# Kernel tuning notes

Hardware: AMD Instinct MI355X
Metric: run time of the kernel (lower is better)

Reference implementation:

```python
import jax, jax.numpy as jnp
import numpy as np

N = 50000   # nodes
E = 200000  # edges
F = 128     # node feat dim
M = 128     # memory dim
FE = 64     # edge feat dim
H = 256     # hidden dim
T = 16      # time encoding dim
O = 64      # output dim
L = 2       # attention layers
NH = 4      # heads
HD = H // NH
SCALE = float(np.sqrt(HD))


def time_enc(t, w, phi):
    # Time2Vec: linear first channel, sinusoidal rest
    wt = t[..., None] * w + phi
    return jnp.concatenate([wt[..., :1], jnp.sin(wt[..., 1:])], axis=-1)


def layer_norm(x, g, b, eps=1e-5):
    m = x.mean(-1, keepdims=True)
    v = jnp.mean((x - m) ** 2, axis=-1, keepdims=True)
    return (x - m) / jnp.sqrt(v + eps) * g + b


def setup_inputs() -> dict:
    key = jax.random.key(0)
    ks = jax.random.split(key, 12)
    s = 0.05  # weight scale for numeric sanity
    return {
        "node_feat": jax.random.normal(ks[0], (N, F), jnp.float32),
        "memory": jax.random.normal(ks[1], (N, M), jnp.float32),
        "edge_index": jax.random.randint(ks[2], (2, E), 0, N),
        "edge_feat": jax.random.normal(ks[3], (E, FE), jnp.float32),
        "edge_times": jax.random.uniform(ks[4], (E,), jnp.float32),
        "in_w": jax.random.normal(ks[5], (H, F + M), jnp.float32) * s,
        "in_b": jnp.zeros((H,), jnp.float32),
        "te_w": jax.random.normal(ks[6], (L, T), jnp.float32),
        "te_phi": jnp.zeros((L, T), jnp.float32),
        "wq_w": jax.random.normal(ks[7], (L, H, H + T), jnp.float32) * s,
        "wq_b": jnp.zeros((L, H), jnp.float32),
        "wk_w": jax.random.normal(ks[8], (L, H, H + FE + T), jnp.float32) * s,
        "wk_b": jnp.zeros((L, H), jnp.float32),
        "wv_w": jax.random.normal(ks[9], (L, H, H + FE + T), jnp.float32) * s,
        "wv_b": jnp.zeros((L, H), jnp.float32),
        "attn_ln_w": jnp.ones((L, H), jnp.float32),
        "attn_ln_b": jnp.zeros((L, H), jnp.float32),
        "ln_w": jnp.ones((L, H), jnp.float32),
        "ln_b": jnp.zeros((L, H), jnp.float32),
        "out_w": jax.random.normal(ks[10], (O, H), jnp.float32) * s,
        "out_b": jnp.zeros((O,), jnp.float32),
    }


def reference(node_feat, memory, edge_index, edge_feat, edge_times,
              in_w, in_b, te_w, te_phi, wq_w, wq_b, wk_w, wk_b, wv_w, wv_b,
              attn_ln_w, attn_ln_b, ln_w, ln_b, out_w, out_b):
    src, dst = edge_index[0], edge_index[1]
    td = 0.0 - edge_times  # query_time = 0.0 (default)
    h = jnp.concatenate([node_feat, memory], axis=-1) @ in_w.T + in_b  # (N, H)
    for l in range(L):
        tenc = time_enc(td, te_w[l], te_phi[l])                       # (E, T)
        h_dst = h[dst]                                                # (E, H)
        msg = jnp.concatenate([h[src], edge_feat, tenc], axis=-1)     # (E, H+FE+T)
        q_te = time_enc(jnp.zeros((N,), h.dtype), te_w[l], te_phi[l]) # (N, T)
        # faithful to source: E > max(dst_ids) so branch is dst_feat[dst_ids]
        q_in = jnp.concatenate([h_dst[dst], q_te[dst]], axis=-1)      # (E, H+T)
        Q = (q_in @ wq_w[l].T + wq_b[l]).reshape(E, NH, HD)
        K = (msg @ wk_w[l].T + wk_b[l]).reshape(E, NH, HD)
        V = msg @ wv_w[l].T + wv_b[l]                                 # (E, H)
        scores = (Q * K).sum(-1) / SCALE                              # (E, NH)
        attn = jnp.exp(jnp.clip(scores, -5.0, 5.0))
        af = attn.mean(-1, keepdims=True)                             # (E, 1)
        agg = jax.ops.segment_sum(V * af, dst, num_segments=N)        # (N, H)
        nrm = jax.ops.segment_sum(af, dst, num_segments=N)            # (N, 1)
        h_new = layer_norm(agg / (nrm + 1e-8), attn_ln_w[l], attn_ln_b[l])
        h = layer_norm(h + h_new, ln_w[l], ln_b[l])
    return jax.nn.gelu(h @ out_w.T + out_b, approximate=False)        # (N, O)
```

## Files before the change

### kernel.cpp

```cpp
#include <hip/hip_runtime.h>
#include <hip/hip_bf16.h>
#include <math.h>

#define NN 50000
#define EE 200000

typedef __bf16 bf16x8 __attribute__((ext_vector_type(8)));
typedef __bf16 bf16x4 __attribute__((ext_vector_type(4)));
typedef __bf16 bf16x2 __attribute__((ext_vector_type(2)));
typedef float f32x4 __attribute__((ext_vector_type(4)));

static __device__ __forceinline__ bf16x8 ld8(const __bf16* p) {
  return *reinterpret_cast<const bf16x8*>(p);
}
static __device__ __forceinline__ bf16x4 ld4(const __bf16* p) {
  return *reinterpret_cast<const bf16x4*>(p);
}
static __device__ __forceinline__ bf16x8 zero8() {
  bf16x8 z;
  #pragma unroll
  for (int j = 0; j < 8; ++j) z[j] = (__bf16)0.0f;
  return z;
}


__global__ __launch_bounds__(256) void k_prep(const float* __restrict__ inw,
                                              const float* __restrict__ wq,
                                              const float* __restrict__ wk,
                                              const float* __restrict__ wvw,
                                              const float* __restrict__ ow,
                                              const float* __restrict__ ef,
                                              const float* __restrict__ tim,
                                              const float* __restrict__ tew,
                                              const float* __restrict__ teph,
                                              const float* __restrict__ wqb,
                                              const int* __restrict__ ei,
                                              __bf16* __restrict__ cinw,
                                              __bf16* __restrict__ cwq,
                                              __bf16* __restrict__ cwk,
                                              __bf16* __restrict__ cwv,
                                              __bf16* __restrict__ cow,
                                              __bf16* __restrict__ twk,
                                              __bf16* __restrict__ aux,
                                              float* __restrict__ cq,
                                              int* __restrict__ cnt) {
  const int b = blockIdx.x;
  if (b < 2208) {
    int i = b * 256 + threadIdx.x;
    if (i < 65536) cinw[i] = (__bf16)inw[i];
    else if (i < 204800) { int j = i - 65536;  cwq[j] = (__bf16)wq[j]; }
    else if (i < 376832) { int j = i - 204800; cwk[j] = (__bf16)wk[j]; }
    else if (i < 548864) { int j = i - 376832; cwv[j] = (__bf16)wvw[j]; }
    else if (i < 565248) { int j = i - 548864; cow[j] = (__bf16)ow[j]; }
  } else if (b < 2400) {
    int i = (b - 2208) * 256 + threadIdx.x;
    int l = i / 24576, r = i % 24576;
    int h = r / 6144, jd = r % 6144;
    int j = jd / 64, d = jd % 64;
    __bf16 v = (__bf16)0.0f;
    if (j < 80) v = (__bf16)wk[((size_t)l * 256 + h * 64 + d) * 336 + 256 + j];
    twk[i] = v;
  } else if (b < 52400) {
    int lane = threadIdx.x & 63;
    int wv = threadIdx.x >> 6;
    int e = (b - 2400) * 4 + wv;
    __bf16* row = aux + (size_t)e * 96;
    row[lane] = (__bf16)ef[(size_t)e * 64 + lane];
    if (lane >= 16 && lane < 32) row[64 + lane] = (__bf16)0.0f;
  } else if (b < 52402) {
    int l = b - 52400;
    int n = threadIdx.x;
    const float* wq_l = wq + (size_t)l * 256 * 272;
    const float* teph_l = teph + l * 16;
    float s = wqb[l * 256 + n];
    for (int t = 0; t < 16; ++t) {
      float ph = teph_l[t];
      float q = (t == 0) ? ph : sinf(ph);
      s += q * wq_l[(size_t)n * 272 + 256 + t];
    }
    cq[l * 256 + n] = s;
  } else if (b < 64902) {
    int idx = (b - 52402) * 256 + threadIdx.x;
    int e = idx >> 4, t = idx & 15;
    float td = -tim[e];
    float wt = td * tew[t] + teph[t];
    float v = (t == 0) ? wt : __sinf(wt);
    aux[(size_t)e * 96 + 64 + t] = (__bf16)v;
  } else {
    int e = (b - 64902) * 256 + threadIdx.x;
    if (e < EE) atomicAdd(&cnt[ei[EE + e]], 1);
  }
}

__global__ __launch_bounds__(256) void k_blksum(const int* __restrict__ wp, int* __restrict__ bsum) {
  __shared__ int red[256];
  int i = blockIdx.x * 256 + threadIdx.x;
  int v = (i < NN) ? wp[i] : 0;
  red[threadIdx.x] = v;
  __syncthreads();
  for (int off = 128; off > 0; off >>= 1) {
    if (threadIdx.x < off) red[threadIdx.x] += red[threadIdx.x + off];
    __syncthreads();
  }
  if (threadIdx.x == 0) bsum[blockIdx.x] = red[0];
}

__global__ __launch_bounds__(256) void k_scanb(int* __restrict__ bsum, int nb) {
  __shared__ int s[256];
  int t = threadIdx.x;
  int v = (t < nb) ? bsum[t] : 0;
  s[t] = v;
  __syncthreads();
  for (int off = 1; off < 256; off <<= 1) {
    int u = (t >= off) ? s[t - off] : 0;
    __syncthreads();
    s[t] += u;
    __syncthreads();
  }
  if (t < nb) bsum[t] = s[t] - v;
}

__global__ __launch_bounds__(256) void k_scanc(int* __restrict__ wp,
                                               const int* __restrict__ bsum,
                                               int* __restrict__ rowptr) {
  __shared__ int s[256];
  int i = blockIdx.x * 256 + threadIdx.x;
  int t = threadIdx.x;
  int v = (i < NN) ? wp[i] : 0;
  s[t] = v;
  __syncthreads();
  for (int off = 1; off < 256; off <<= 1) {
    int u = (t >= off) ? s[t - off] : 0;
    __syncthreads();
    s[t] += u;
    __syncthreads();
  }
  int excl = s[t] - v + bsum[blockIdx.x];
  if (i < NN) { rowptr[i] = excl; wp[i] = excl; }
  if (i == 0) rowptr[NN] = EE;
}

__global__ __launch_bounds__(256) void k_fill(const int* __restrict__ ei,
                                              int* __restrict__ wp,
                                              int* __restrict__ bucket) {
  int e = blockIdx.x * 256 + threadIdx.x;
  if (e < EE) {
    int d = ei[EE + e];
    int pos = atomicAdd(&wp[d], 1);
    bucket[pos] = e;
  }
}

__global__ __launch_bounds__(256) void k_auxte(const float* __restrict__ tim,
                                               const float* __restrict__ tew_l,
                                               const float* __restrict__ teph_l,
                                               __bf16* __restrict__ aux) {
  int idx = blockIdx.x * 256 + threadIdx.x;
  int e = idx >> 4, t = idx & 15;
  float td = -tim[e];
  float wt = td * tew_l[t] + teph_l[t];
  float v = (t == 0) ? wt : __sinf(wt);
  aux[(size_t)e * 96 + 64 + t] = (__bf16)v;
}


__global__ __launch_bounds__(256) void k_h0(const float* __restrict__ nf,
                                            const float* __restrict__ mem,
                                            const __bf16* __restrict__ w,
                                            const float* __restrict__ bias,
                                            __bf16* __restrict__ hb) {
  __shared__ __bf16 As[64][264];
  const int t = threadIdx.x;
  const int lane = t & 63;
  const int wv = t >> 6;
  const int c = lane & 15, g = lane >> 4;
  const int row0 = blockIdx.x * 64;
  const int colbase = wv * 64;

  {
    const int col4 = t & 63;
    const int rb = t >> 6;
    const bool useMem = (col4 >= 32);
    const int coff = (useMem ? (col4 - 32) : col4) * 4;
    const float* basep = useMem ? mem : nf;
    #pragma unroll
    for (int i = 0; i < 16; ++i) {
      const int row = rb + i * 4;
      int grow = row0 + row; if (grow >= NN) grow = NN - 1;
      f32x4 v = *reinterpret_cast<const f32x4*>(basep + (size_t)grow * 128 + coff);
      bf16x4 bv;
      bv[0] = (__bf16)v[0]; bv[1] = (__bf16)v[1];
      bv[2] = (__bf16)v[2]; bv[3] = (__bf16)v[3];
      *reinterpret_cast<bf16x4*>(&As[row][col4 * 4]) = bv;
    }
  }
  __syncthreads();

  const __bf16* Bp[4];
  #pragma unroll
  for (int ct = 0; ct < 4; ++ct)
    Bp[ct] = w + (size_t)(colbase + ct * 16 + c) * 256;

  f32x4 acc[4][4];
  #pragma unroll
  for (int rt = 0; rt < 4; ++rt)
    for (int ct = 0; ct < 4; ++ct)
      for (int r = 0; r < 4; ++r) acc[rt][ct][r] = 0.0f;

  #pragma unroll
  for (int ks = 0; ks < 8; ++ks) {
    const int k = ks * 32 + g * 8;
    bf16x8 a[4], b[4];
    #pragma unroll
    for (int rt = 0; rt < 4; ++rt)
      a[rt] = *reinterpret_cast<const bf16x8*>(&As[rt * 16 + c][k]);
    #pragma unroll
    for (int ct = 0; ct < 4; ++ct) b[ct] = ld8(Bp[ct] + k);
    #pragma unroll
    for (int rt = 0; rt < 4; ++rt)
      #pragma unroll
      for (int ct = 0; ct < 4; ++ct)
        acc[rt][ct] = __builtin_amdgcn_mfma_f32_16x16x32_bf16(a[rt], b[ct], acc[rt][ct], 0, 0, 0);
  }
  __syncthreads();

  #pragma unroll
  for (int ct = 0; ct < 4; ++ct) {
    const float bv = bias[colbase + ct * 16 + c];
    #pragma unroll
    for (int rt = 0; rt < 4; ++rt)
      #pragma unroll
      for (int rr = 0; rr < 4; ++rr)
        As[rt * 16 + g * 4 + rr][colbase + ct * 16 + c] = (__bf16)(acc[rt][ct][rr] + bv);
  }
  #pragma unroll
  for (int i = 0; i < 8; ++i) {
    const int r = i * 8 + (lane >> 3);
    const int ck = lane & 7;
    bf16x8 v = *reinterpret_cast<const bf16x8*>(&As[r][colbase + ck * 8]);
    const int row = row0 + r;
    if (row < NN)
      *reinterpret_cast<bf16x8*>(hb + (size_t)row * 256 + colbase + ck * 8) = v;
  }
}


__global__ __launch_bounds__(256, 2) void k_qkn(const __bf16* __restrict__ hb,
                                                const __bf16* __restrict__ wq_l,
                                                const __bf16* __restrict__ wk_l,
                                                const float* __restrict__ cq,
                                                const float* __restrict__ bk_l,
                                                const __bf16* __restrict__ twk_l,
                                                __bf16* __restrict__ Qn,
                                                __bf16* __restrict__ Kn,
                                                __bf16* __restrict__ G) {
  __shared__ __bf16 As[64][264];
  __shared__ __bf16 tile[4][64][84];
  const int lane = threadIdx.x & 63;
  const int wv = threadIdx.x >> 6;
  const int c = lane & 15, g = lane >> 4;
  const int row0 = blockIdx.x * 64;
  const int colbase = wv * 64;

  {
    #pragma unroll
    for (int i = 0; i < 8; ++i) {
      const int cc = threadIdx.x + i * 256;
      const int row = cc >> 5;
      const int col8 = cc & 31;
      int grow = row0 + row; if (grow >= NN) grow = NN - 1;
      *reinterpret_cast<bf16x8*>(&As[row][col8 * 8]) =
          ld8(hb + (size_t)grow * 256 + col8 * 8);
    }
  }
  __syncthreads();

  f32x4 acc[4][4];

  #pragma unroll
  for (int rt = 0; rt < 4; ++rt)
    for (int ct = 0; ct < 4; ++ct)
      for (int r = 0; r < 4; ++r) acc[rt][ct][r] = 0.0f;
  {
    const __bf16* Bp[4];
    #pragma unroll
    for (int ct = 0; ct < 4; ++ct)
      Bp[ct] = wq_l + (size_t)(colbase + ct * 16 + c) * 272;
    #pragma unroll
    for (int ks = 0; ks < 8; ++ks) {
      const int k = ks * 32 + g * 8;
      bf16x8 a[4], b[4];
      #pragma unroll
      for (int rt = 0; rt < 4; ++rt)
        a[rt] = *reinterpret_cast<const bf16x8*>(&As[rt * 16 + c][k]);
      #pragma unroll
      for (int ct = 0; ct < 4; ++ct) b[ct] = ld8(Bp[ct] + k);
      #pragma unroll
      for (int rt = 0; rt < 4; ++rt)
        #pragma unroll
        for (int ct = 0; ct < 4; ++ct)
          acc[rt][ct] = __builtin_amdgcn_mfma_f32_16x16x32_bf16(a[rt], b[ct], acc[rt][ct], 0, 0, 0);
    }
  }
  #pragma unroll
  for (int ct = 0; ct < 4; ++ct) {
    const float cqv = cq[colbase + ct * 16 + c];
    #pragma unroll
    for (int rt = 0; rt < 4; ++rt)
      #pragma unroll
      for (int rr = 0; rr < 4; ++rr)
        tile[wv][rt * 16 + g * 4 + rr][ct * 16 + c] = (__bf16)(acc[rt][ct][rr] + cqv);
  }
  #pragma unroll
  for (int i = 0; i < 8; ++i) {
    const int r = i * 8 + (lane >> 3);
    const int ck = lane & 7;
    bf16x8 v = *reinterpret_cast<const bf16x8*>(&tile[wv][r][ck * 8]);
    const int row = row0 + r;
    if (row < NN)
      *reinterpret_cast<bf16x8*>(Qn + (size_t)row * 256 + colbase + ck * 8) = v;
  }

  {
    f32x4 accg[4][5];
    #pragma unroll
    for (int rt = 0; rt < 4; ++rt)
      for (int ct = 0; ct < 5; ++ct)
        for (int r = 0; r < 4; ++r) accg[rt][ct][r] = 0.0f;
    const __bf16* Bp[5];
    #pragma unroll
    for (int ct = 0; ct < 5; ++ct)
      Bp[ct] = twk_l + (size_t)wv * 6144 + (size_t)(ct * 16 + c) * 64;
    #pragma unroll
    for (int ks = 0; ks < 2; ++ks) {
      const int k = ks * 32 + g * 8;
      bf16x8 a[4], b[5];
      #pragma unroll
      for (int rt = 0; rt < 4; ++rt)
        a[rt] = *reinterpret_cast<const bf16x8*>(&tile[wv][rt * 16 + c][k]);
      #pragma unroll
      for (int ct = 0; ct < 5; ++ct) b[ct] = ld8(Bp[ct] + k);
      #pragma unroll
      for (int rt = 0; rt < 4; ++rt)
        #pragma unroll
        for (int ct = 0; ct < 5; ++ct)
          accg[rt][ct] = __builtin_amdgcn_mfma_f32_16x16x32_bf16(a[rt], b[ct], accg[rt][ct], 0, 0, 0);
    }
    #pragma unroll
    for (int ct = 0; ct < 5; ++ct) {
      #pragma unroll
      for (int rt = 0; rt < 4; ++rt)
        #pragma unroll
        for (int rr = 0; rr < 4; ++rr)
          tile[wv][rt * 16 + g * 4 + rr][ct * 16 + c] = (__bf16)accg[rt][ct][rr];
    }
    #pragma unroll
    for (int i = 0; i < 10; ++i) {
      const int idx = i * 64 + lane;
      const int r = idx / 10;
      const int ck = idx % 10;
      bf16x8 v = *reinterpret_cast<const bf16x8*>(&tile[wv][r][ck * 8]);
      const int row = row0 + r;
      if (row < NN)
        *reinterpret_cast<bf16x8*>(G + (size_t)row * 320 + wv * 80 + ck * 8) = v;
    }
  }

  #pragma unroll
  for (int rt = 0; rt < 4; ++rt)
    for (int ct = 0; ct < 4; ++ct)
      for (int r = 0; r < 4; ++r) acc[rt][ct][r] = 0.0f;
  {
    const __bf16* Bp[4];
    #pragma unroll
    for (int ct = 0; ct < 4; ++ct)
      Bp[ct] = wk_l + (size_t)(colbase + ct * 16 + c) * 336;
    #pragma unroll
    for (int ks = 0; ks < 8; ++ks) {
      const int k = ks * 32 + g * 8;
      bf16x8 a[4], b[4];
      #pragma unroll
      for (int rt = 0; rt < 4; ++rt)
        a[rt] = *reinterpret_cast<const bf16x8*>(&As[rt * 16 + c][k]);
      #pragma unroll
      for (int ct = 0; ct < 4; ++ct) b[ct] = ld8(Bp[ct] + k);
      #pragma unroll
      for (int rt = 0; rt < 4; ++rt)
        #pragma unroll
        for (int ct = 0; ct < 4; ++ct)
          acc[rt][ct] = __builtin_amdgcn_mfma_f32_16x16x32_bf16(a[rt], b[ct], acc[rt][ct], 0, 0, 0);
    }
  }
  #pragma unroll
  for (int ct = 0; ct < 4; ++ct) {
    const float bkv = bk_l[colbase + ct * 16 + c];
    #pragma unroll
    for (int rt = 0; rt < 4; ++rt)
      #pragma unroll
      for (int rr = 0; rr < 4; ++rr)
        tile[wv][rt * 16 + g * 4 + rr][ct * 16 + c] = (__bf16)(acc[rt][ct][rr] + bkv);
  }
  #pragma unroll
  for (int i = 0; i < 8; ++i) {
    const int r = i * 8 + (lane >> 3);
    const int ck = lane & 7;
    bf16x8 v = *reinterpret_cast<const bf16x8*>(&tile[wv][r][ck * 8]);
    const int row = row0 + r;
    if (row < NN)
      *reinterpret_cast<bf16x8*>(Kn + (size_t)row * 256 + colbase + ck * 8) = v;
  }
}


__global__ __launch_bounds__(256, 4) void k_sagg(const __bf16* __restrict__ hb,
                                                 const __bf16* __restrict__ aux,
                                                 const __bf16* __restrict__ G,
                                                 const __bf16* __restrict__ Qn,
                                                 const __bf16* __restrict__ Kn,
                                                 const int* __restrict__ ei,
                                                 const int* __restrict__ rowptr,
                                                 const int* __restrict__ bucket,
                                                 __bf16* __restrict__ maggH,
                                                 __bf16* __restrict__ maggX,
                                                 float* __restrict__ sfac) {
  const int lane = threadIdx.x & 63;
  const int wv = threadIdx.x >> 6;
  const int node = blockIdx.x * 4 + wv;
  const int beg = rowptr[node], end = rowptr[node + 1];
  const int c = lane & 15;
  const int grp = lane >> 4;

  float aH[4] = {0, 0, 0, 0};
  float aXv[4] = {0, 0, 0, 0};
  float aXs = 0.0f;
  float nrm = 0.0f;

  if (beg < end) {
    const int iq = ei[EE + node];
    const __bf16* Qr = Qn + (size_t)iq * 256;
    const __bf16* Gr = G + (size_t)iq * 320;

    bf16x4 qv = ld4(Qr + lane * 4);
    bf16x4 gv = ld4(Gr + grp * 80 + c * 4);
    const float gs = (float)Gr[grp * 80 + 64 + c];

    int e = bucket[beg];
    int s = ei[e];
    bf16x4 kv = ld4(Kn + (size_t)s * 256 + lane * 4);
    bf16x4 hv = ld4(hb + (size_t)s * 256 + lane * 4);
    bf16x4 av = ld4(aux + (size_t)e * 96 + c * 4);
    float as = (float)aux[(size_t)e * 96 + 64 + c];

    for (int i = beg; i < end; ++i) {
      const int en = (i + 1 < end) ? bucket[i + 1] : e;
      const int sn = ei[en];
      bf16x4 kv_n = ld4(Kn + (size_t)sn * 256 + lane * 4);
      bf16x4 hv_n = ld4(hb + (size_t)sn * 256 + lane * 4);
      bf16x4 av_n = ld4(aux + (size_t)en * 96 + c * 4);
      float as_n = (float)aux[(size_t)en * 96 + 64 + c];

      float p = gs * as;
      #pragma unroll
      for (int j = 0; j < 4; ++j) {
        p += (float)qv[j] * (float)kv[j];
        p += (float)gv[j] * (float)av[j];
      }
      p += __shfl_xor(p, 1, 64);
      p += __shfl_xor(p, 2, 64);
      p += __shfl_xor(p, 4, 64);
      p += __shfl_xor(p, 8, 64);
      float sc = fminf(5.0f, fmaxf(-5.0f, p * 0.125f));
      float ex = __expf(sc);
      ex += __shfl_xor(ex, 16, 64);
      ex += __shfl_xor(ex, 32, 64);
      const float a = ex * 0.25f;

      nrm += a;
      #pragma unroll
      for (int j = 0; j < 4; ++j) aH[j] += a * (float)hv[j];
      if (grp == 0) {
        #pragma unroll
        for (int j = 0; j < 4; ++j) aXv[j] += a * (float)av[j];
      } else if (grp == 1) {
        aXs += a * as;
      }
      kv = kv_n; hv = hv_n; av = av_n; as = as_n; e = en;
    }
  }

  const float inv = 1.0f / (nrm + 1e-8f);
  bf16x4 oh;
  #pragma unroll
  for (int j = 0; j < 4; ++j) oh[j] = (__bf16)(aH[j] * inv);
  *reinterpret_cast<bf16x4*>(maggH + (size_t)node * 256 + lane * 4) = oh;
  if (grp == 0) {
    bf16x4 ox;
    #pragma unroll
    for (int j = 0; j < 4; ++j) ox[j] = (__bf16)(aXv[j] * inv);
    *reinterpret_cast<bf16x4*>(maggX + (size_t)node * 96 + c * 4) = ox;
  } else if (grp == 1) {
    maggX[(size_t)node * 96 + 64 + c] = (__bf16)(aXs * inv);
  } else if (grp == 2) {
    maggX[(size_t)node * 96 + 80 + c] = (__bf16)0.0f;
  }
  if (lane == 0) sfac[node] = nrm * inv;
}


__global__ __launch_bounds__(256, 4) void k_score3(const __bf16* __restrict__ aux,
                                                   const __bf16* __restrict__ G,
                                                   const __bf16* __restrict__ Qn,
                                                   const __bf16* __restrict__ Kn,
                                                   const int* __restrict__ ei,
                                                   const int* __restrict__ rowptr,
                                                   const int* __restrict__ bucket,
                                                   float* __restrict__ af) {
  const int lane = threadIdx.x & 63;
  const int wv = threadIdx.x >> 6;
  const int node = blockIdx.x * 4 + wv;
  const int beg = rowptr[node], end = rowptr[node + 1];
  const int c = lane & 15;
  const int grp = lane >> 4;

  if (beg < end) {
    const int iq = ei[EE + node];
    const __bf16* Qr = Qn + (size_t)iq * 256;
    const __bf16* Gr = G + (size_t)iq * 320;

    bf16x4 qv = ld4(Qr + lane * 4);
    bf16x4 gv = ld4(Gr + grp * 80 + c * 4);
    const float gs = (float)Gr[grp * 80 + 64 + c];

    int e = bucket[beg];
    int s = ei[e];
    for (int i = beg; i < end; ++i) {
      const int en = (i + 1 < end) ? bucket[i + 1] : e;
      const int sn = ei[en];
      bf16x4 kv = ld4(Kn + (size_t)s * 256 + lane * 4);
      bf16x4 av = ld4(aux + (size_t)e * 96 + c * 4);
      float as = (float)aux[(size_t)e * 96 + 64 + c];

      float p = gs * as;
      #pragma unroll
      for (int j = 0; j < 4; ++j) {
        p += (float)qv[j] * (float)kv[j];
        p += (float)gv[j] * (float)av[j];
      }
      p += __shfl_xor(p, 1, 64);
      p += __shfl_xor(p, 2, 64);
      p += __shfl_xor(p, 4, 64);
      p += __shfl_xor(p, 8, 64);
      float sc = fminf(5.0f, fmaxf(-5.0f, p * 0.125f));
      float ex = __expf(sc);
      ex += __shfl_xor(ex, 16, 64);
      ex += __shfl_xor(ex, 32, 64);
      if (lane == 0) af[e] = ex * 0.25f;
      e = en; s = sn;
    }
  }
}

__global__ __launch_bounds__(256, 4) void k_magg(const __bf16* __restrict__ hb,
                                                 const __bf16* __restrict__ aux,
                                                 const int* __restrict__ ei,
                                                 const int* __restrict__ rowptr,
                                                 const int* __restrict__ bucket,
                                                 const float* __restrict__ af,
                                                 __bf16* __restrict__ maggH,
                                                 __bf16* __restrict__ maggX,
                                                 float* __restrict__ sfac) {
  const int lane = threadIdx.x & 63;
  const int wv = threadIdx.x >> 6;
  const int node = blockIdx.x * 4 + wv;
  const int beg = rowptr[node], end = rowptr[node + 1];

  float aH[4] = {0, 0, 0, 0};
  float aX[2] = {0, 0};
  float nrm = 0.0f;
  if (beg < end) {
    int e = bucket[beg];
    float a = af[e];
    int s = ei[e];
    for (int i = beg; i < end; ++i) {
      const int en = (i + 1 < end) ? bucket[i + 1] : e;
      const float an = af[en];
      const int sn = ei[en];
      bf16x4 hv = ld4(hb + (size_t)s * 256 + lane * 4);
      #pragma unroll
      for (int j = 0; j < 4; ++j) aH[j] += a * (float)hv[j];
      if (lane < 48) {
        bf16x2 xv = *reinterpret_cast<const bf16x2*>(aux + (size_t)e * 96 + lane * 2);
        aX[0] += a * (float)xv[0];
        aX[1] += a * (float)xv[1];
      }
      nrm += a;
      e = en; a = an; s = sn;
    }
  }
  const float inv = 1.0f / (nrm + 1e-8f);
  bf16x4 oh;
  #pragma unroll
  for (int j = 0; j < 4; ++j) oh[j] = (__bf16)(aH[j] * inv);
  *reinterpret_cast<bf16x4*>(maggH + (size_t)node * 256 + lane * 4) = oh;
  if (lane < 48) {
    bf16x2 ox;
    ox[0] = (__bf16)(aX[0] * inv);
    ox[1] = (__bf16)(aX[1] * inv);
    *reinterpret_cast<bf16x2*>(maggX + (size_t)node * 96 + lane * 2) = ox;
  }
  if (lane == 0) sfac[node] = nrm * inv;
}


__global__ __launch_bounds__(256, 3) void k_vnorm(const __bf16* __restrict__ maggH,
                                                  const __bf16* __restrict__ maggX,
                                                  const float* __restrict__ sfac,
                                                  const __bf16* __restrict__ wv_l,
                                                  const float* __restrict__ bv_l,
                                                  __bf16* __restrict__ hb,
                                                  const float* __restrict__ aw,
                                                  const float* __restrict__ ab,
                                                  const float* __restrict__ lw,
                                                  const float* __restrict__ lb) {
  __shared__ __bf16 tile[4][64][68];
  __shared__ float redA[64][4];
  __shared__ float redB[64][4];
  const int lane = threadIdx.x & 63;
  const int wv = threadIdx.x >> 6;
  const int c = lane & 15, g = lane >> 4;
  const int row0 = blockIdx.x * 64;
  const int colbase = wv * 64;

  #pragma unroll
  for (int i = 0; i < 8; ++i) {
    const int r = i * 8 + (lane >> 3);
    const int ck = lane & 7;
    int row = row0 + r; if (row >= NN) row = NN - 1;
    *reinterpret_cast<bf16x8*>(&tile[wv][r][ck * 8]) =
        ld8(hb + (size_t)row * 256 + colbase + ck * 8);
  }

  const __bf16* AH[4];
  const __bf16* AX[4];
  const __bf16* Bp[4];
  #pragma unroll
  for (int rt = 0; rt < 4; ++rt) {
    int r = row0 + rt * 16 + c; if (r >= NN) r = NN - 1;
    AH[rt] = maggH + (size_t)r * 256;
    AX[rt] = maggX + (size_t)r * 96;
  }
  #pragma unroll
  for (int ct = 0; ct < 4; ++ct)
    Bp[ct] = wv_l + (size_t)(colbase + ct * 16 + c) * 336;

  f32x4 acc[4][4];
  #pragma unroll
  for (int rt = 0; rt < 4; ++rt)
    for (int ct = 0; ct < 4; ++ct)
      for (int r = 0; r < 4; ++r) acc[rt][ct][r] = 0.0f;

  for (int ks = 0; ks < 8; ++ks) {
    const int k = ks * 32 + g * 8;
    bf16x8 a[4], b[4];
    #pragma unroll
    for (int rt = 0; rt < 4; ++rt) a[rt] = ld8(AH[rt] + k);
    #pragma unroll
    for (int ct = 0; ct < 4; ++ct) b[ct] = ld8(Bp[ct] + k);
    #pragma unroll
    for (int rt = 0; rt < 4; ++rt)
      #pragma unroll
      for (int ct = 0; ct < 4; ++ct)
        acc[rt][ct] = __builtin_amdgcn_mfma_f32_16x16x32_bf16(a[rt], b[ct], acc[rt][ct], 0, 0, 0);
  }
  const bf16x8 bz = zero8();
  for (int ks = 0; ks < 3; ++ks) {
    const int kk = ks * 32 + g * 8;
    bf16x8 a[4], b[4];
    #pragma unroll
    for (int rt = 0; rt < 4; ++rt) a[rt] = ld8(AX[rt] + kk);
    #pragma unroll
    for (int ct = 0; ct < 4; ++ct)
      b[ct] = (kk < 80) ? ld8(Bp[ct] + 256 + kk) : bz;
    #pragma unroll
    for (int rt = 0; rt < 4; ++rt)
      #pragma unroll
      for (int ct = 0; ct < 4; ++ct)
        acc[rt][ct] = __builtin_amdgcn_mfma_f32_16x16x32_bf16(a[rt], b[ct], acc[rt][ct], 0, 0, 0);
  }

  float sf[4][4];
  #pragma unroll
  for (int rt = 0; rt < 4; ++rt)
    #pragma unroll
    for (int rr = 0; rr < 4; ++rr) {
      int row = row0 + rt * 16 + g * 4 + rr; if (row >= NN) row = NN - 1;
      sf[rt][rr] = sfac[row];
    }
  float bvv[4], awv[4], abv[4], lwv[4], lbv[4];
  #pragma unroll
  for (int ct = 0; ct < 4; ++ct) {
    const int col = colbase + ct * 16 + c;
    bvv[ct] = bv_l[col];
    awv[ct] = aw[col]; abv[ct] = ab[col];
    lwv[ct] = lw[col]; lbv[ct] = lb[col];
  }
  #pragma unroll
  for (int rt = 0; rt < 4; ++rt)
    #pragma unroll
    for (int ct = 0; ct < 4; ++ct)
      #pragma unroll
      for (int rr = 0; rr < 4; ++rr)
        acc[rt][ct][rr] += sf[rt][rr] * bvv[ct];

  float s1[4][4];
  #pragma unroll
  for (int rt = 0; rt < 4; ++rt)
    #pragma unroll
    for (int rr = 0; rr < 4; ++rr) {
      float s = 0.0f;
      #pragma unroll
      for (int ct = 0; ct < 4; ++ct) s += acc[rt][ct][rr];
      #pragma unroll
      for (int m = 1; m < 16; m <<= 1) s += __shfl_xor(s, m, 64);
      s1[rt][rr] = s;
    }
  if (c == 0)
    #pragma unroll
    for (int rt = 0; rt < 4; ++rt)
      #pragma unroll
      for (int rr = 0; rr < 4; ++rr)
        redA[rt * 16 + g * 4 + rr][wv] = s1[rt][rr];
  __syncthreads();
  float mean1[4][4];
  #pragma unroll
  for (int rt = 0; rt < 4; ++rt)
    #pragma unroll
    for (int rr = 0; rr < 4; ++rr) {
      const int r = rt * 16 + g * 4 + rr;
      mean1[rt][rr] = (redA[r][0] + redA[r][1] + redA[r][2] + redA[r][3]) * (1.0f / 256.0f);
    }
  #pragma unroll
  for (int rt = 0; rt < 4; ++rt)
    #pragma unroll
    for (int rr = 0; rr < 4; ++rr) {
      float q = 0.0f;
      #pragma unroll
      for (int ct = 0; ct < 4; ++ct) {
        float d = acc[rt][ct][rr] - mean1[rt][rr];
        q += d * d;
      }
      #pragma unroll
      for (int m = 1; m < 16; m <<= 1) q += __shfl_xor(q, m, 64);
      s1[rt][rr] = q;
    }
  if (c == 0)
    #pragma unroll
    for (int rt = 0; rt < 4; ++rt)
      #pragma unroll
      for (int rr = 0; rr < 4; ++rr)
        redB[rt * 16 + g * 4 + rr][wv] = s1[rt][rr];
  __syncthreads();
  float rstd1[4][4];
  #pragma unroll
  for (int rt = 0; rt < 4; ++rt)
    #pragma unroll
    for (int rr = 0; rr < 4; ++rr) {
      const int r = rt * 16 + g * 4 + rr;
      float v = (redB[r][0] + redB[r][1] + redB[r][2] + redB[r][3]) * (1.0f / 256.0f);
      rstd1[rt][rr] = rsqrtf(v + 1e-5f);
    }

  #pragma unroll
  for (int rt = 0; rt < 4; ++rt)
    #pragma unroll
    for (int rr = 0; rr < 4; ++rr) {
      const int r = rt * 16 + g * 4 + rr;
      float s = 0.0f;
      #pragma unroll
      for (int ct = 0; ct < 4; ++ct) {
        float hbv = (float)tile[wv][r][ct * 16 + c];
        float y = hbv + (acc[rt][ct][rr] - mean1[rt][rr]) * rstd1[rt][rr] * awv[ct] + abv[ct];
        acc[rt][ct][rr] = y;
        s += y;
      }
      #pragma unroll
      for (int m = 1; m < 16; m <<= 1) s += __shfl_xor(s, m, 64);
      s1[rt][rr] = s;
    }
  if (c == 0)
    #pragma unroll
    for (int rt = 0; rt < 4; ++rt)
      #pragma unroll
      for (int rr = 0; rr < 4; ++rr)
        redA[rt * 16 + g * 4 + rr][wv] = s1[rt][rr];
  __syncthreads();
  float mean2[4][4];
  #pragma unroll
  for (int rt = 0; rt < 4; ++rt)
    #pragma unroll
    for (int rr = 0; rr < 4; ++rr) {
      const int r = rt * 16 + g * 4 + rr;
      mean2[rt][rr] = (redA[r][0] + redA[r][1] + redA[r][2] + redA[r][3]) * (1.0f / 256.0f);
    }
  #pragma unroll
  for (int rt = 0; rt < 4; ++rt)
    #pragma unroll
    for (int rr = 0; rr < 4; ++rr) {
      float q = 0.0f;
      #pragma unroll
      for (int ct = 0; ct < 4; ++ct) {
        float d = acc[rt][ct][rr] - mean2[rt][rr];
        q += d * d;
      }
      #pragma unroll
      for (int m = 1; m < 16; m <<= 1) q += __shfl_xor(q, m, 64);
      s1[rt][rr] = q;
    }
  if (c == 0)
    #pragma unroll
    for (int rt = 0; rt < 4; ++rt)
      #pragma unroll
      for (int rr = 0; rr < 4; ++rr)
        redB[rt * 16 + g * 4 + rr][wv] = s1[rt][rr];
  __syncthreads();
  #pragma unroll
  for (int rt = 0; rt < 4; ++rt)
    #pragma unroll
    for (int rr = 0; rr < 4; ++rr) {
      const int r = rt * 16 + g * 4 + rr;
      float v = (redB[r][0] + redB[r][1] + redB[r][2] + redB[r][3]) * (1.0f / 256.0f);
      const float rstd2 = rsqrtf(v + 1e-5f);
      #pragma unroll
      for (int ct = 0; ct < 4; ++ct)
        tile[wv][r][ct * 16 + c] =
            (__bf16)((acc[rt][ct][rr] - mean2[rt][rr]) * rstd2 * lwv[ct] + lbv[ct]);
    }

  #pragma unroll
  for (int i = 0; i < 8; ++i) {
    const int r = i * 8 + (lane >> 3);
    const int ck = lane & 7;
    bf16x8 v = *reinterpret_cast<const bf16x8*>(&tile[wv][r][ck * 8]);
    const int row = row0 + r;
    if (row < NN)
      *reinterpret_cast<bf16x8*>(hb + (size_t)row * 256 + colbase + ck * 8) = v;
  }
}


__global__ __launch_bounds__(256, 4) void k_out(const __bf16* __restrict__ hb,
                                                const __bf16* __restrict__ ow,
                                                const float* __restrict__ ob,
                                                float* __restrict__ out) {
  const int lane = threadIdx.x & 63;
  const int wv = threadIdx.x >> 6;
  const int c = lane & 15, g = lane >> 4;
  const int row0 = blockIdx.x * 64 + wv * 16;

  int r = row0 + c; if (r >= NN) r = NN - 1;
  const __bf16* Ar = hb + (size_t)r * 256;
  const __bf16* Bp[4];
  #pragma unroll
  for (int ct = 0; ct < 4; ++ct)
    Bp[ct] = ow + (size_t)(ct * 16 + c) * 256;

  f32x4 acc[4];
  #pragma unroll
  for (int ct = 0; ct < 4; ++ct)
    for (int rr = 0; rr < 4; ++rr) acc[ct][rr] = 0.0f;

  for (int ks = 0; ks < 8; ++ks) {
    const int k = ks * 32 + g * 8;
    bf16x8 a = ld8(Ar + k);
    bf16x8 b[4];
    #pragma unroll
    for (int ct = 0; ct < 4; ++ct) b[ct] = ld8(Bp[ct] + k);
    #pragma unroll
    for (int ct = 0; ct < 4; ++ct)
      acc[ct] = __builtin_amdgcn_mfma_f32_16x16x32_bf16(a, b[ct], acc[ct], 0, 0, 0);
  }
  #pragma unroll
  for (int ct = 0; ct < 4; ++ct) {
    const int col = ct * 16 + c;
    const float bv = ob[col];
    #pragma unroll
    for (int rr = 0; rr < 4; ++rr) {
      const int row = row0 + g * 4 + rr;
      if (row < NN) {
        float x = acc[ct][rr] + bv;
        out[(size_t)row * 64 + col] = 0.5f * x * (1.0f + erff(x * 0.70710678118654752f));
      }
    }
  }
}


extern "C" void kernel_launch(void* const* d_in, const int* in_sizes, int n_in,
                              void* d_out, int out_size, void* d_ws, size_t ws_size,
                              hipStream_t stream) {
  (void)in_sizes; (void)n_in; (void)out_size;
  const float* nf   = (const float*)d_in[0];
  const float* mem  = (const float*)d_in[1];
  const int*   ei   = (const int*)d_in[2];
  const float* ef   = (const float*)d_in[3];
  const float* tim  = (const float*)d_in[4];
  const float* inw  = (const float*)d_in[5];
  const float* inb  = (const float*)d_in[6];
  const float* tew  = (const float*)d_in[7];
  const float* teph = (const float*)d_in[8];
  const float* wq   = (const float*)d_in[9];
  const float* wqb  = (const float*)d_in[10];
  const float* wk   = (const float*)d_in[11];
  const float* wkb  = (const float*)d_in[12];
  const float* wvw  = (const float*)d_in[13];
  const float* wvb  = (const float*)d_in[14];
  const float* alw  = (const float*)d_in[15];
  const float* alb  = (const float*)d_in[16];
  const float* lnw  = (const float*)d_in[17];
  const float* lnb  = (const float*)d_in[18];
  const float* ow   = (const float*)d_in[19];
  const float* ob   = (const float*)d_in[20];
  float* out = (float*)d_out;

  char* ws = (char*)d_ws;
  const bool big = ws_size >= 186700000ULL;

  __bf16* hb    = (__bf16*)(ws + 0);
  __bf16* aux   = (__bf16*)(ws + 25600000);
  __bf16* Qn    = (__bf16*)(ws + 64000000);
  __bf16* Kn    = (__bf16*)(ws + 89600000);
  __bf16* G     = (__bf16*)(ws + 115200000);
  __bf16* maggH = (__bf16*)(ws + (big ? 147200000 : 115200000));
  __bf16* maggX = (__bf16*)(ws + (big ? 172800000 : 140800000));
  const size_t o_tail = big ? 182400000 : 150400000;
  float*  sfac  = (float*) (ws + o_tail);
  float*  af    = (float*) (ws + o_tail + 200000);
  int*    rowptr= (int*)   (ws + o_tail + 1800000);
  int*    wp    = (int*)   (ws + o_tail + 2000192);
  int*    bucket= (int*)   (ws + o_tail + 2200192);
  float*  cq    = (float*) (ws + o_tail + 3000192);
  int*    bsum  = (int*)   (ws + o_tail + 3002240);
  __bf16* cinw  = (__bf16*)(ws + o_tail + 3003264);
  __bf16* cwq   = (__bf16*)(ws + o_tail + 3134336);
  __bf16* cwk   = (__bf16*)(ws + o_tail + 3412864);
  __bf16* cwv   = (__bf16*)(ws + o_tail + 3756928);
  __bf16* cow   = (__bf16*)(ws + o_tail + 4100992);
  __bf16* twk   = (__bf16*)(ws + o_tail + 4133760);

  const int NB = (NN + 255) / 256;
  hipMemsetAsync(wp, 0, NN * 4, stream);
  k_prep<<<65684, 256, 0, stream>>>(inw, wq, wk, wvw, ow, ef, tim, tew, teph, wqb, ei,
                                    cinw, cwq, cwk, cwv, cow, twk, aux, cq, wp);
  k_blksum<<<NB, 256, 0, stream>>>(wp, bsum);
  k_scanb<<<1, 256, 0, stream>>>(bsum, NB);
  k_scanc<<<NB, 256, 0, stream>>>(wp, bsum, rowptr);
  k_fill<<<(EE + 255) / 256, 256, 0, stream>>>(ei, wp, bucket);

  k_h0<<<(NN + 63) / 64, 256, 0, stream>>>(nf, mem, cinw, inb, hb);

  for (int l = 0; l < 2; ++l) {
    const __bf16* wq_l = cwq + (size_t)l * 256 * 272;
    const __bf16* wk_l = cwk + (size_t)l * 256 * 336;
    const __bf16* wv_l = cwv + (size_t)l * 256 * 336;
    if (l > 0)
      k_auxte<<<EE * 16 / 256, 256, 0, stream>>>(tim, tew + l * 16, teph + l * 16, aux);
    k_qkn<<<(NN + 63) / 64, 256, 0, stream>>>(hb, wq_l, wk_l, cq + l * 256, wkb + l * 256,
                                              twk + (size_t)l * 24576, Qn, Kn, G);
    if (big) {
      k_sagg<<<NN / 4, 256, 0, stream>>>(hb, aux, G, Qn, Kn, ei, rowptr, bucket,
                                         maggH, maggX, sfac);
    } else {
      k_score3<<<NN / 4, 256, 0, stream>>>(aux, G, Qn, Kn, ei, rowptr, bucket, af);
      k_magg<<<NN / 4, 256, 0, stream>>>(hb, aux, ei, rowptr, bucket, af, maggH, maggX, sfac);
    }
    k_vnorm<<<(NN + 63) / 64, 256, 0, stream>>>(maggH, maggX, sfac, wv_l, wvb + l * 256, hb,
                                                alw + l * 256, alb + l * 256,
                                                lnw + l * 256, lnb + l * 256);
  }
  k_out<<<(NN + 63) / 64, 256, 0, stream>>>(hb, cow, ob, out);
}
```

Baseline: 566.7 us.

## Unroll edge aggregation by four and fuse output projection into final vnorm

The per-node edge loop in k_sagg now handles four edges per iteration. All gathers for those four edges are issued together and their shuffle reductions are interleaved, which exposes more memory-level parallelism than the previous one-ahead prefetch. The occupancy hint on k_sagg's launch bounds is dropped. The final output projection with GELU is fused into the last-layer k_vnorm, reading the normalized tile from shared memory; this removes the hb write-back, a kernel launch and the re-read. The trade-off is higher register pressure in k_sagg and wasted work on padded edges for nodes with low degree.

```diff
diff --git a/kernel.cpp b/kernel.cpp
--- a/kernel.cpp
+++ b/kernel.cpp
@@ -412,17 +412,17 @@
 }
 
 
-__global__ __launch_bounds__(256, 4) void k_sagg(const __bf16* __restrict__ hb,
-                                                 const __bf16* __restrict__ aux,
-                                                 const __bf16* __restrict__ G,
-                                                 const __bf16* __restrict__ Qn,
-                                                 const __bf16* __restrict__ Kn,
-                                                 const int* __restrict__ ei,
-                                                 const int* __restrict__ rowptr,
-                                                 const int* __restrict__ bucket,
-                                                 __bf16* __restrict__ maggH,
-                                                 __bf16* __restrict__ maggX,
-                                                 float* __restrict__ sfac) {
+__global__ __launch_bounds__(256) void k_sagg(const __bf16* __restrict__ hb,
+                                              const __bf16* __restrict__ aux,
+                                              const __bf16* __restrict__ G,
+                                              const __bf16* __restrict__ Qn,
+                                              const __bf16* __restrict__ Kn,
+                                              const int* __restrict__ ei,
+                                              const int* __restrict__ rowptr,
+                                              const int* __restrict__ bucket,
+                                              __bf16* __restrict__ maggH,
+                                              __bf16* __restrict__ maggX,
+                                              float* __restrict__ sfac) {
   const int lane = threadIdx.x & 63;
   const int wv = threadIdx.x >> 6;
   const int node = blockIdx.x * 4 + wv;
@@ -444,47 +444,78 @@
     bf16x4 gv = ld4(Gr + grp * 80 + c * 4);
     const float gs = (float)Gr[grp * 80 + 64 + c];
 
-    int e = bucket[beg];
-    int s = ei[e];
-    bf16x4 kv = ld4(Kn + (size_t)s * 256 + lane * 4);
-    bf16x4 hv = ld4(hb + (size_t)s * 256 + lane * 4);
-    bf16x4 av = ld4(aux + (size_t)e * 96 + c * 4);
-    float as = (float)aux[(size_t)e * 96 + 64 + c];
-
-    for (int i = beg; i < end; ++i) {
-      const int en = (i + 1 < end) ? bucket[i + 1] : e;
-      const int sn = ei[en];
-      bf16x4 kv_n = ld4(Kn + (size_t)sn * 256 + lane * 4);
-      bf16x4 hv_n = ld4(hb + (size_t)sn * 256 + lane * 4);
-      bf16x4 av_n = ld4(aux + (size_t)en * 96 + c * 4);
-      float as_n = (float)aux[(size_t)en * 96 + 64 + c];
-
-      float p = gs * as;
+    for (int base = beg; base < end; base += 4) {
+      const int rem = end - base;
+      const int iA = base;
+      const int iB = base + ((1 < rem) ? 1 : 0);
+      const int iC = base + ((2 < rem) ? 2 : 0);
+      const int iD = base + ((3 < rem) ? 3 : 0);
+      const int eA = bucket[iA], eB = bucket[iB], eC = bucket[iC], eD = bucket[iD];
+      const int sA = ei[eA], sB = ei[eB], sC = ei[eC], sD = ei[eD];
+
+      bf16x4 kvA = ld4(Kn + (size_t)sA * 256 + lane * 4);
+      bf16x4 kvB = ld4(Kn + (size_t)sB * 256 + lane * 4);
+      bf16x4 kvC = ld4(Kn + (size_t)sC * 256 + lane * 4);
+      bf16x4 kvD = ld4(Kn + (size_t)sD * 256 + lane * 4);
+      bf16x4 hvA = ld4(hb + (size_t)sA * 256 + lane * 4);
+      bf16x4 hvB = ld4(hb + (size_t)sB * 256 + lane * 4);
+      bf16x4 hvC = ld4(hb + (size_t)sC * 256 + lane * 4);
+      bf16x4 hvD = ld4(hb + (size_t)sD * 256 + lane * 4);
+      bf16x4 avA = ld4(aux + (size_t)eA * 96 + c * 4);
+      bf16x4 avB = ld4(aux + (size_t)eB * 96 + c * 4);
+      bf16x4 avC = ld4(aux + (size_t)eC * 96 + c * 4);
+      bf16x4 avD = ld4(aux + (size_t)eD * 96 + c * 4);
+      const float asA = (float)aux[(size_t)eA * 96 + 64 + c];
+      const float asB = (float)aux[(size_t)eB * 96 + 64 + c];
+      const float asC = (float)aux[(size_t)eC * 96 + 64 + c];
+      const float asD = (float)aux[(size_t)eD * 96 + 64 + c];
+
+      float pA = gs * asA, pB = gs * asB, pC = gs * asC, pD = gs * asD;
       #pragma unroll
       for (int j = 0; j < 4; ++j) {
-        p += (float)qv[j] * (float)kv[j];
-        p += (float)gv[j] * (float)av[j];
+        const float qj = (float)qv[j], gj = (float)gv[j];
+        pA += qj * (float)kvA[j] + gj * (float)avA[j];
+        pB += qj * (float)kvB[j] + gj * (float)avB[j];
+        pC += qj * (float)kvC[j] + gj * (float)avC[j];
+        pD += qj * (float)kvD[j] + gj * (float)avD[j];
       }
-      p += __shfl_xor(p, 1, 64);
-      p += __shfl_xor(p, 2, 64);
-      p += __shfl_xor(p, 4, 64);
-      p += __shfl_xor(p, 8, 64);
-      float sc = fminf(5.0f, fmaxf(-5.0f, p * 0.125f));
-      float ex = __expf(sc);
-      ex += __shfl_xor(ex, 16, 64);
-      ex += __shfl_xor(ex, 32, 64);
-      const float a = ex * 0.25f;
-
-      nrm += a;
-      #pragma unroll
-      for (int j = 0; j < 4; ++j) aH[j] += a * (float)hv[j];
+      #pragma unroll
+      for (int m = 1; m <= 8; m <<= 1) {
+        pA += __shfl_xor(pA, m, 64);
+        pB += __shfl_xor(pB, m, 64);
+        pC += __shfl_xor(pC, m, 64);
+        pD += __shfl_xor(pD, m, 64);
+      }
+      float exA = __expf(fminf(5.0f, fmaxf(-5.0f, pA * 0.125f)));
+      float exB = __expf(fminf(5.0f, fmaxf(-5.0f, pB * 0.125f)));
+      float exC = __expf(fminf(5.0f, fmaxf(-5.0f, pC * 0.125f)));
+      float exD = __expf(fminf(5.0f, fmaxf(-5.0f, pD * 0.125f)));
+      exA += __shfl_xor(exA, 16, 64);
+      exB += __shfl_xor(exB, 16, 64);
+      exC += __shfl_xor(exC, 16, 64);
+      exD += __shfl_xor(exD, 16, 64);
+      exA += __shfl_xor(exA, 32, 64);
+      exB += __shfl_xor(exB, 32, 64);
+      exC += __shfl_xor(exC, 32, 64);
+      exD += __shfl_xor(exD, 32, 64);
+      const float aA = exA * 0.25f;
+      const float aB = (1 < rem) ? exB * 0.25f : 0.0f;
+      const float aC = (2 < rem) ? exC * 0.25f : 0.0f;
+      const float aD = (3 < rem) ? exD * 0.25f : 0.0f;
+
+      nrm += aA + aB + aC + aD;
+      #pragma unroll
+      for (int j = 0; j < 4; ++j)
+        aH[j] += aA * (float)hvA[j] + aB * (float)hvB[j] +
+                 aC * (float)hvC[j] + aD * (float)hvD[j];
       if (grp == 0) {
         #pragma unroll
-        for (int j = 0; j < 4; ++j) aXv[j] += a * (float)av[j];
+        for (int j = 0; j < 4; ++j)
+          aXv[j] += aA * (float)avA[j] + aB * (float)avB[j] +
+                    aC * (float)avC[j] + aD * (float)avD[j];
       } else if (grp == 1) {
-        aXs += a * as;
+        aXs += aA * asA + aB * asB + aC * asC + aD * asD;
       }
-      kv = kv_n; hv = hv_n; av = av_n; as = as_n; e = en;
     }
   }
 
@@ -621,7 +652,11 @@
                                                   const float* __restrict__ aw,
                                                   const float* __restrict__ ab,
                                                   const float* __restrict__ lw,
-                                                  const float* __restrict__ lb) {
+                                                  const float* __restrict__ lb,
+                                                  const __bf16* __restrict__ cow,
+                                                  const float* __restrict__ obias,
+                                                  float* __restrict__ outp,
+                                                  int last) {
   __shared__ __bf16 tile[4][64][68];
   __shared__ float redA[64][4];
   __shared__ float redB[64][4];
@@ -836,61 +871,46 @@
             (__bf16)((acc[rt][ct][rr] - mean2[rt][rr]) * rstd2 * lwv[ct] + lbv[ct]);
     }
 
-  #pragma unroll
-  for (int i = 0; i < 8; ++i) {
-    const int r = i * 8 + (lane >> 3);
-    const int ck = lane & 7;
-    bf16x8 v = *reinterpret_cast<const bf16x8*>(&tile[wv][r][ck * 8]);
-    const int row = row0 + r;
-    if (row < NN)
-      *reinterpret_cast<bf16x8*>(hb + (size_t)row * 256 + colbase + ck * 8) = v;
-  }
-}
-
-
-__global__ __launch_bounds__(256, 4) void k_out(const __bf16* __restrict__ hb,
-                                                const __bf16* __restrict__ ow,
-                                                const float* __restrict__ ob,
-                                                float* __restrict__ out) {
-  const int lane = threadIdx.x & 63;
-  const int wv = threadIdx.x >> 6;
-  const int c = lane & 15, g = lane >> 4;
-  const int row0 = blockIdx.x * 64 + wv * 16;
-
-  int r = row0 + c; if (r >= NN) r = NN - 1;
-  const __bf16* Ar = hb + (size_t)r * 256;
-  const __bf16* Bp[4];
-  #pragma unroll
-  for (int ct = 0; ct < 4; ++ct)
-    Bp[ct] = ow + (size_t)(ct * 16 + c) * 256;
-
-  f32x4 acc[4];
-  #pragma unroll
-  for (int ct = 0; ct < 4; ++ct)
-    for (int rr = 0; rr < 4; ++rr) acc[ct][rr] = 0.0f;
-
-  for (int ks = 0; ks < 8; ++ks) {
-    const int k = ks * 32 + g * 8;
-    bf16x8 a = ld8(Ar + k);
-    bf16x8 b[4];
-    #pragma unroll
-    for (int ct = 0; ct < 4; ++ct) b[ct] = ld8(Bp[ct] + k);
-    #pragma unroll
-    for (int ct = 0; ct < 4; ++ct)
-      acc[ct] = __builtin_amdgcn_mfma_f32_16x16x32_bf16(a, b[ct], acc[ct], 0, 0, 0);
-  }
-  #pragma unroll
-  for (int ct = 0; ct < 4; ++ct) {
-    const int col = ct * 16 + c;
-    const float bv = ob[col];
-    #pragma unroll
-    for (int rr = 0; rr < 4; ++rr) {
-      const int row = row0 + g * 4 + rr;
-      if (row < NN) {
-        float x = acc[ct][rr] + bv;
-        out[(size_t)row * 64 + col] = 0.5f * x * (1.0f + erff(x * 0.70710678118654752f));
+  if (!last) {
+    #pragma unroll
+    for (int i = 0; i < 8; ++i) {
+      const int r = i * 8 + (lane >> 3);
+      const int ck = lane & 7;
+      bf16x8 v = *reinterpret_cast<const bf16x8*>(&tile[wv][r][ck * 8]);
+      const int row = row0 + r;
+      if (row < NN)
+        *reinterpret_cast<bf16x8*>(hb + (size_t)row * 256 + colbase + ck * 8) = v;
+    }
+  } else {
+    __syncthreads();
+    const __bf16* Bop = cow + (size_t)(wv * 16 + c) * 256;
+    f32x4 acc2[4];
+    #pragma unroll
+    for (int rt = 0; rt < 4; ++rt)
+      for (int rr = 0; rr < 4; ++rr) acc2[rt][rr] = 0.0f;
+    #pragma unroll
+    for (int ks = 0; ks < 8; ++ks) {
+      const int k = ks * 32 + g * 8;
+      bf16x8 bfrag = ld8(Bop + k);
+      #pragma unroll
+      for (int rt = 0; rt < 4; ++rt) {
+        bf16x8 afrag = *reinterpret_cast<const bf16x8*>(
+            &tile[ks >> 1][rt * 16 + c][(ks & 1) * 32 + g * 8]);
+        acc2[rt] = __builtin_amdgcn_mfma_f32_16x16x32_bf16(afrag, bfrag, acc2[rt], 0, 0, 0);
       }
     }
+    const int col = wv * 16 + c;
+    const float bo = obias[col];
+    #pragma unroll
+    for (int rt = 0; rt < 4; ++rt)
+      #pragma unroll
+      for (int rr = 0; rr < 4; ++rr) {
+        const int row = row0 + rt * 16 + g * 4 + rr;
+        if (row < NN) {
+          float x = acc2[rt][rr] + bo;
+          outp[(size_t)row * 64 + col] = 0.5f * x * (1.0f + erff(x * 0.70710678118654752f));
+        }
+      }
   }
 }
 
@@ -975,7 +995,7 @@
     }
     k_vnorm<<<(NN + 63) / 64, 256, 0, stream>>>(maggH, maggX, sfac, wv_l, wvb + l * 256, hb,
                                                 alw + l * 256, alb + l * 256,
-                                                lnw + l * 256, lnb + l * 256);
-  }
-  k_out<<<(NN + 63) / 64, 256, 0, stream>>>(hb, cow, ob, out);
-}
+                                                lnw + l * 256, lnb + l * 256,
+                                                cow, ob, out, (l == 1) ? 1 : 0);
+  }
+}
```

After: 566.6 us. Within noise of the previous version (-0.0%).
